# Optimization experiments

Hardware: AMD Instinct MI355X
Metric: run time of the kernel (lower is better)

The kernel has to match this reference:

```python
import jax, jax.numpy as jnp
import numpy as np

B, N, E, H = 4, 2048, 768, 8
D = E // H
SCALING = D ** (-0.5)


def setup_inputs() -> dict:
    key = jax.random.key(0)
    k0, k1, k2, k3, k4 = jax.random.split(key, 5)
    x = jax.random.normal(k0, (B, N, E), dtype=jnp.float32)
    Wqkv = jax.random.normal(k1, (E, 3 * E), dtype=jnp.float32) * 0.02
    bqkv = jax.random.normal(k2, (3 * E,), dtype=jnp.float32) * 0.02
    Wproj = jax.random.normal(k3, (E, E), dtype=jnp.float32) * 0.02
    bproj = jax.random.normal(k4, (E,), dtype=jnp.float32) * 0.02
    return {"x": x, "Wqkv": Wqkv, "bqkv": bqkv, "Wproj": Wproj, "bproj": bproj}


def reference(x, Wqkv, bqkv, Wproj, bproj):
    b, n, e = x.shape
    h, d = H, E // H
    # QKV projection: [b, n, 3e]
    qkv = x @ Wqkv + bqkv
    # rearrange 'b n (h d qkv) -> qkv b h n d': qkv is the INNERMOST axis
    qkv = qkv.reshape(b, n, h, d, 3)
    q = jnp.transpose(qkv[..., 0], (0, 2, 1, 3))  # [b, h, n, d]
    k = jnp.transpose(qkv[..., 1], (0, 2, 1, 3))
    v = jnp.transpose(qkv[..., 2], (0, 2, 1, 3))
    # unscaled attention scores, softmax, then post-softmax scaling (as in source)
    energy = jnp.einsum('bhqd,bhkd->bhqk', q, k)  # [b, h, n, n]
    att = jax.nn.softmax(energy, axis=-1) * SCALING
    out = jnp.einsum('bhqk,bhkd->bhqd', att, v)   # [b, h, n, d]
    out = jnp.transpose(out, (0, 2, 1, 3)).reshape(b, n, e)
    return out @ Wproj + bproj
```

## Files before the change

### kernel.cpp

```cpp
#include <hip/hip_runtime.h>
#include <cstdint>

#define BB 4
#define SEQ 2048
#define EMB 768
#define NH 8
#define HD 96
#define E3 2304
#define MTOK 8192
#define SCALING 0.10206207261596575f
#define LOG2E 1.44269504f

typedef unsigned short u16;
typedef unsigned int u32;
typedef __bf16 bf16x8 __attribute__((ext_vector_type(8)));
typedef float f32x4 __attribute__((ext_vector_type(4)));
typedef float f32x16 __attribute__((ext_vector_type(16)));

__device__ __forceinline__ u16 f2bf(float f) {
    union { float f; uint32_t u; } c; c.f = f;
    uint32_t u = c.u;
    return (u16)((u + 0x7FFFu + ((u >> 16) & 1u)) >> 16);
}
__device__ __forceinline__ u16 f2bf_fast(float f) {
    union { float f; uint32_t u; } c; c.f = f;
    return (u16)((c.u + 0x8000u) >> 16);
}
__device__ __forceinline__ uint32_t pk2(float a, float b) {
    return (uint32_t)f2bf(a) | ((uint32_t)f2bf(b) << 16);
}
__device__ __forceinline__ uint32_t pk2_fast(float a, float b) {
    return (uint32_t)f2bf_fast(a) | ((uint32_t)f2bf_fast(b) << 16);
}
__device__ __forceinline__ float fexp2(float x) {
    return __builtin_amdgcn_exp2f(x);
}
__device__ __forceinline__ void async16(const u16* g, u16* l) {
    __builtin_amdgcn_global_load_lds(
        (const __attribute__((address_space(1))) void*)g,
        (__attribute__((address_space(3))) void*)l, 16, 0, 0);
}


__global__ void cvt_x_kernel(const float* __restrict__ src, u16* __restrict__ dst, int n8) {
    int i = blockIdx.x * blockDim.x + threadIdx.x;
    if (i >= n8) return;
    const float4* s4 = (const float4*)src;
    float4 a = s4[2 * i];
    float4 c = s4[2 * i + 1];
    uint4 o;
    o.x = pk2(a.x, a.y); o.y = pk2(a.z, a.w);
    o.z = pk2(c.x, c.y); o.w = pk2(c.z, c.w);
    ((uint4*)dst)[i] = o;
}

__global__ __launch_bounds__(256) void transpose_w_kernel(const float* __restrict__ src,
                                                          u16* __restrict__ dst,
                                                          int ncols, int mode) {
    __shared__ float T[64][65];
    int j0 = blockIdx.x * 64, k0 = blockIdx.y * 64;
    int tid = threadIdx.x;
#pragma unroll
    for (int it = 0; it < 16; ++it) {
        int lin = it * 256 + tid;
        int rr2 = lin >> 6, jj = lin & 63;
        int j = j0 + jj;
        int c;
        if (mode == 0) c = j;
        else if (mode == 1) { int s = j / 768, rr = j % 768; c = (rr / 96) * 288 + (rr % 96) * 3 + s; }
        else { c = (j / 96) * 288 + (j % 96) * 3 + 2; }
        T[rr2][jj] = src[(k0 + rr2) * ncols + c];
    }
    __syncthreads();
#pragma unroll
    for (int it = 0; it < 16; ++it) {
        int lin = it * 256 + tid;
        int jr = lin >> 6, kc = lin & 63;
        dst[(size_t)(j0 + jr) * 768 + k0 + kc] = f2bf(T[kc][jr]);
    }
}


__device__ __forceinline__ void gemm_tiles(const u16* __restrict__ A,
                                           const u16* __restrict__ Bt,
                                           int m0, int n0, int tid,
                                           u16* As, u16* Bs, f32x4 acc[4][4]) {
    const int lane = tid & 63;
    const int w = tid >> 6;
    const int l15 = lane & 15;
    const int quad = lane >> 4;
    const int wr = (w >> 1) * 64;
    const int wc = (w & 1) * 64;
    const int swz = l15 & 7;
    for (int kb = 0; kb < 768; kb += 64) {
#pragma unroll
        for (int it = 0; it < 4; ++it) {
            int base = (w * 4 + it) * 64;
            int lin = base + lane;
            int row = lin >> 3, cl = lin & 7;
            int cg = cl ^ (row & 7);
            async16(&A[(size_t)(m0 + row) * 768 + kb + cg * 8], &As[base * 8]);
            async16(&Bt[(size_t)(n0 + row) * 768 + kb + cg * 8], &Bs[base * 8]);
        }
        __syncthreads();
#pragma unroll
        for (int ks = 0; ks < 2; ++ks) {
            bf16x8 af[4], bfg[4];
#pragma unroll
            for (int fi = 0; fi < 4; ++fi)
                af[fi] = *(const bf16x8*)&As[(wr + fi * 16 + l15) * 64 + (((ks * 4 + quad) ^ swz) * 8)];
#pragma unroll
            for (int fj = 0; fj < 4; ++fj)
                bfg[fj] = *(const bf16x8*)&Bs[(wc + fj * 16 + l15) * 64 + (((ks * 4 + quad) ^ swz) * 8)];
#pragma unroll
            for (int fi = 0; fi < 4; ++fi)
#pragma unroll
                for (int fj = 0; fj < 4; ++fj)
                    acc[fi][fj] = __builtin_amdgcn_mfma_f32_16x16x32_bf16(af[fi], bfg[fj], acc[fi][fj], 0, 0, 0);
        }
        __syncthreads();
    }
}

__global__ __launch_bounds__(256) void gemm_qk_kernel(const u16* __restrict__ A,
                                                      const u16* __restrict__ Bt,
                                                      const float* __restrict__ bqkv,
                                                      u16* __restrict__ qb,
                                                      u16* __restrict__ kg) {
    __shared__ __align__(16) u16 As[128 * 64];
    __shared__ __align__(16) u16 Bs[128 * 64];
    int tid = threadIdx.x;
    int n0 = blockIdx.x * 128, m0 = blockIdx.y * 128;
    f32x4 acc[4][4] = {};
    gemm_tiles(A, Bt, m0, n0, tid, As, Bs, acc);
    int lane = tid & 63, w = tid >> 6, l15 = lane & 15, quad = lane >> 4;
    int wr = (w >> 1) * 64, wc = (w & 1) * 64;
#pragma unroll
    for (int fj = 0; fj < 4; ++fj) {
        int j = n0 + wc + fj * 16 + l15;
        int s = j / 768, rr = j % 768;
        int hh = rr / 96, dd = rr % 96;
        float bv = bqkv[hh * 288 + dd * 3 + s];
#pragma unroll
        for (int fi = 0; fi < 4; ++fi) {
#pragma unroll
            for (int r = 0; r < 4; ++r) {
                int m = m0 + wr + fi * 16 + quad * 4 + r;
                int b = m >> 11, n = m & 2047;
                int bh = b * NH + hh;
                float v = acc[fi][fj][r] + bv;
                if (s == 0) {
                    qb[((size_t)bh * SEQ + n) * HD + dd] = f2bf(v * LOG2E);
                } else {
                    int cp = (dd >> 3) ^ (n & 7);
                    kg[((size_t)bh * SEQ + n) * 128 + cp * 8 + (dd & 7)] = f2bf(v);
                }
            }
        }
    }
}

__global__ __launch_bounds__(256) void gemm_v_kernel(const u16* __restrict__ A,
                                                     const u16* __restrict__ Bt,
                                                     const float* __restrict__ bqkv,
                                                     u16* __restrict__ vt) {
    __shared__ __align__(16) u16 As[128 * 64];
    __shared__ __align__(16) u16 Bs[128 * 64];
    int tid = threadIdx.x;
    int n0 = blockIdx.x * 128, m0 = blockIdx.y * 128;
    f32x4 acc[4][4] = {};
    gemm_tiles(A, Bt, m0, n0, tid, As, Bs, acc);
    int lane = tid & 63, w = tid >> 6, l15 = lane & 15, quad = lane >> 4;
    int wr = (w >> 1) * 64, wc = (w & 1) * 64;
    float bvs[4][4]; int hhs[4][4], dds[4][4];
#pragma unroll
    for (int fi = 0; fi < 4; ++fi)
#pragma unroll
        for (int r = 0; r < 4; ++r) {
            int m = m0 + wr + fi * 16 + quad * 4 + r;
            int hh = m / 96, dd = m % 96;
            hhs[fi][r] = hh; dds[fi][r] = dd;
            bvs[fi][r] = bqkv[hh * 288 + dd * 3 + 2];
        }
#pragma unroll
    for (int fj = 0; fj < 4; ++fj) {
        int n = n0 + wc + fj * 16 + l15;
        int b = n >> 11, nn = n & 2047;
#pragma unroll
        for (int fi = 0; fi < 4; ++fi) {
#pragma unroll
            for (int r = 0; r < 4; ++r) {
                int dd = dds[fi][r];
                int kk = (nn & ~63) | ((((nn >> 3) ^ dd) & 7) << 3) | (nn & 7);
                vt[((size_t)(b * NH + hhs[fi][r]) * HD + dd) * SEQ + kk] =
                    f2bf(acc[fi][fj][r] + bvs[fi][r]);
            }
        }
    }
}

__global__ __launch_bounds__(256) void gemm_proj_kernel(const u16* __restrict__ A,
                                                        const u16* __restrict__ Bt,
                                                        const float* __restrict__ bias,
                                                        float* __restrict__ out) {
    __shared__ __align__(16) u16 As[128 * 64];
    __shared__ __align__(16) u16 Bs[128 * 64];
    int tid = threadIdx.x;
    int n0 = blockIdx.x * 128, m0 = blockIdx.y * 128;
    f32x4 acc[4][4] = {};
    gemm_tiles(A, Bt, m0, n0, tid, As, Bs, acc);
    int lane = tid & 63, w = tid >> 6, l15 = lane & 15, quad = lane >> 4;
    int wr = (w >> 1) * 64, wc = (w & 1) * 64;
#pragma unroll
    for (int fj = 0; fj < 4; ++fj) {
        int j = n0 + wc + fj * 16 + l15;
        float bv = bias[j];
#pragma unroll
        for (int fi = 0; fi < 4; ++fi) {
#pragma unroll
            for (int r = 0; r < 4; ++r) {
                int m = m0 + wr + fi * 16 + quad * 4 + r;
                out[(size_t)m * 768 + j] = acc[fi][fj][r] + bv;
            }
        }
    }
}

__global__ __launch_bounds__(256) void attn_kernel(const u16* __restrict__ Q,
                                                   const u16* __restrict__ Kg,
                                                   const u16* __restrict__ Vt,
                                                   u16* __restrict__ AO) {
    __shared__ __align__(16) u16 Ks[2][64 * 128];
    __shared__ __align__(16) u16 Vs[2][96 * 64];
    int tid = threadIdx.x;
    int lane = tid & 63, w = tid >> 6;
    int l31 = lane & 31, hf = lane >> 5;
    int swz = l31 & 7;
    int qt = blockIdx.x, bh = blockIdx.y;
    int b = bh >> 3, head = bh & 7;
    const u16* qp = Q + (size_t)bh * SEQ * HD;
    const u16* kgp = Kg + (size_t)bh * SEQ * 128;
    const u16* vtp = Vt + (size_t)bh * HD * SEQ;
    int q0 = qt * 128 + w * 32;

    bf16x8 aq[6];
#pragma unroll
    for (int dc = 0; dc < 6; ++dc)
        aq[dc] = *(const bf16x8*)&qp[(size_t)(q0 + l31) * HD + dc * 16 + hf * 8];

    f32x16 Ot[3] = {};
    float lp = 0.f;

    auto stage = [&](int kt, int buf) {
        int k0 = kt * 64;
#pragma unroll
        for (int it = 0; it < 4; ++it) {
            int cw = w * 4 + it;
            async16(kgp + (size_t)(k0 + cw * 4 + (lane >> 4)) * 128 + (lane & 15) * 8,
                    &Ks[buf][cw * 512]);
        }
#pragma unroll
        for (int it = 0; it < 3; ++it) {
            int vw = w * 3 + it;
            async16(vtp + (size_t)(vw * 8 + (lane >> 3)) * SEQ + k0 + (lane & 7) * 8,
                    &Vs[buf][vw * 512]);
        }
    };

    stage(0, 0);
    __syncthreads();

    for (int kt = 0; kt < SEQ / 64; ++kt) {
        int cur = kt & 1;
        if (kt + 1 < SEQ / 64) stage(kt + 1, cur ^ 1);

        f32x16 Sv[2] = {};
#pragma unroll
        for (int tau = 0; tau < 2; ++tau) {
#pragma unroll
            for (int dc = 0; dc < 6; ++dc) {
                bf16x8 ka = *(const bf16x8*)&Ks[cur][(tau * 32 + l31) * 128 + (((2 * dc + hf) ^ swz) * 8)];
                Sv[tau] = __builtin_amdgcn_mfma_f32_32x32x16_bf16(ka, aq[dc], Sv[tau], 0, 0, 0);
            }
        }

        u32 pk[2][4][2];
#pragma unroll
        for (int tau = 0; tau < 2; ++tau)
#pragma unroll
            for (int g = 0; g < 4; ++g)
#pragma unroll
                for (int u = 0; u < 2; ++u) {
                    float p0 = fexp2(Sv[tau][g * 4 + 2 * u]);
                    float p1 = fexp2(Sv[tau][g * 4 + 2 * u + 1]);
                    lp += p0 + p1;
                    pk[tau][g][u] = pk2_fast(p0, p1);
                }
        u32 rv[2][2][2];
#pragma unroll
        for (int tau = 0; tau < 2; ++tau)
#pragma unroll
            for (int kc = 0; kc < 2; ++kc)
#pragma unroll
                for (int u = 0; u < 2; ++u) {
                    u32 send = hf ? pk[tau][2 * kc][u] : pk[tau][2 * kc + 1][u];
                    rv[tau][kc][u] = (u32)__shfl_xor((int)send, 32);
                }
#pragma unroll
        for (int tau = 0; tau < 2; ++tau) {
#pragma unroll
            for (int kc = 0; kc < 2; ++kc) {
                union { u32 u[4]; bf16x8 v; } pf;
                pf.u[0] = hf ? rv[tau][kc][0] : pk[tau][2 * kc][0];
                pf.u[1] = hf ? rv[tau][kc][1] : pk[tau][2 * kc][1];
                pf.u[2] = hf ? pk[tau][2 * kc + 1][0] : rv[tau][kc][0];
                pf.u[3] = hf ? pk[tau][2 * kc + 1][1] : rv[tau][kc][1];
#pragma unroll
                for (int t = 0; t < 3; ++t) {
                    bf16x8 va = *(const bf16x8*)&Vs[cur][(t * 32 + l31) * 64 + (((4 * tau + 2 * kc + hf) ^ swz) * 8)];
                    Ot[t] = __builtin_amdgcn_mfma_f32_32x32x16_bf16(va, pf.v, Ot[t], 0, 0, 0);
                }
            }
        }
        __syncthreads();
    }

    float l = lp + __shfl_xor(lp, 32);
    float sc = SCALING / l;
    int n = q0 + l31;
    size_t rowbase = ((size_t)b * SEQ + n) * EMB + head * HD;
#pragma unroll
    for (int t = 0; t < 3; ++t) {
#pragma unroll
        for (int g = 0; g < 4; ++g) {
            int d0 = t * 32 + 8 * g + 4 * hf;
            uint2 val;
            val.x = pk2(Ot[t][g * 4 + 0] * sc, Ot[t][g * 4 + 1] * sc);
            val.y = pk2(Ot[t][g * 4 + 2] * sc, Ot[t][g * 4 + 3] * sc);
            *(uint2*)&AO[rowbase + d0] = val;
        }
    }
}


extern "C" void kernel_launch(void* const* d_in, const int* in_sizes, int n_in,
                              void* d_out, int out_size, void* d_ws, size_t ws_size,
                              hipStream_t stream) {
    const float* x     = (const float*)d_in[0];
    const float* Wqkv  = (const float*)d_in[1];
    const float* bqkv  = (const float*)d_in[2];
    const float* Wproj = (const float*)d_in[3];
    const float* bproj = (const float*)d_in[4];
    float* out = (float*)d_out;

    char* p = (char*)d_ws;
    u16*   xb   = (u16*)p;  p += (size_t)MTOK * EMB * 2;
    u16*   wqkT = (u16*)p;  p += (size_t)1536 * EMB * 2;
    u16*   wvr  = (u16*)p;  p += (size_t)EMB * EMB * 2;
    u16*   wpt  = (u16*)p;  p += (size_t)EMB * EMB * 2;
    u16*   qb   = (u16*)p;  p += (size_t)MTOK * EMB * 2;
    u16*   kg   = (u16*)p;  p += (size_t)BB * NH * SEQ * 128 * 2;
    u16*   vt   = (u16*)p;  p += (size_t)MTOK * EMB * 2;
    u16*   ao   = (u16*)p;  p += (size_t)MTOK * EMB * 2;

    cvt_x_kernel<<<MTOK * EMB / 8 / 256, 256, 0, stream>>>(x, xb, MTOK * EMB / 8);
    transpose_w_kernel<<<dim3(1536 / 64, EMB / 64), 256, 0, stream>>>(Wqkv, wqkT, E3, 1);
    transpose_w_kernel<<<dim3(EMB / 64, EMB / 64), 256, 0, stream>>>(Wqkv, wvr, E3, 2);
    transpose_w_kernel<<<dim3(EMB / 64, EMB / 64), 256, 0, stream>>>(Wproj, wpt, EMB, 0);
    gemm_qk_kernel<<<dim3(1536 / 128, MTOK / 128), 256, 0, stream>>>(xb, wqkT, bqkv, qb, kg);
    gemm_v_kernel<<<dim3(MTOK / 128, EMB / 128), 256, 0, stream>>>(wvr, xb, bqkv, vt);
    attn_kernel<<<dim3(SEQ / 128, BB * NH), 256, 0, stream>>>(qb, kg, vt, ao);
    gemm_proj_kernel<<<dim3(EMB / 128, MTOK / 128), 256, 0, stream>>>(ao, wpt, bproj, out);
}
```

Before: 255.5 us.

## Split attention over key halves with combine pass, double query rows per warp

The attention kernel now handles 64 query rows per warp, so each K fragment load feeds two score MFMAs and each V load feeds two output MFMAs. The key range is split into two halves across blockIdx.z, giving a split-K flash layout whose bf16 partial outputs and row sums are merged and normalized by a new combine kernel. The V-projection and output-projection GEMMs move to 128x64 tiles to launch more blocks. The aim is higher LDS reuse and more parallelism in attention, at the cost of extra partial-output traffic, one more launch, and higher register pressure under launch_bounds(256,2).

```diff
diff --git a/kernel.cpp b/kernel.cpp
--- a/kernel.cpp
+++ b/kernel.cpp
@@ -8,6 +8,7 @@
 #define HD 96
 #define E3 2304
 #define MTOK 8192
+#define NROWS 65536
 #define SCALING 0.10206207261596575f
 #define LOG2E 1.44269504f
 
@@ -31,6 +32,9 @@
 }
 __device__ __forceinline__ uint32_t pk2_fast(float a, float b) {
     return (uint32_t)f2bf_fast(a) | ((uint32_t)f2bf_fast(b) << 16);
+}
+__device__ __forceinline__ float bf2f(u16 h) {
+    union { uint32_t u; float f; } c; c.u = ((uint32_t)h) << 16; return c.f;
 }
 __device__ __forceinline__ float fexp2(float x) {
     return __builtin_amdgcn_exp2f(x);
@@ -116,6 +120,54 @@
             for (int fi = 0; fi < 4; ++fi)
 #pragma unroll
                 for (int fj = 0; fj < 4; ++fj)
+                    acc[fi][fj] = __builtin_amdgcn_mfma_f32_16x16x32_bf16(af[fi], bfg[fj], acc[fi][fj], 0, 0, 0);
+        }
+        __syncthreads();
+    }
+}
+
+__device__ __forceinline__ void gemm_tiles64(const u16* __restrict__ A,
+                                             const u16* __restrict__ Bt,
+                                             int m0, int n0, int tid,
+                                             u16* As, u16* Bs, f32x4 acc[4][2]) {
+    const int lane = tid & 63;
+    const int w = tid >> 6;
+    const int l15 = lane & 15;
+    const int quad = lane >> 4;
+    const int wr = (w >> 1) * 64;
+    const int wc = (w & 1) * 32;
+    const int swz = l15 & 7;
+    for (int kb = 0; kb < 768; kb += 64) {
+#pragma unroll
+        for (int it = 0; it < 4; ++it) {
+            int base = (w * 4 + it) * 64;
+            int lin = base + lane;
+            int row = lin >> 3, cl = lin & 7;
+            int cg = cl ^ (row & 7);
+            async16(&A[(size_t)(m0 + row) * 768 + kb + cg * 8], &As[base * 8]);
+        }
+#pragma unroll
+        for (int it = 0; it < 2; ++it) {
+            int base = (w * 2 + it) * 64;
+            int lin = base + lane;
+            int row = lin >> 3, cl = lin & 7;
+            int cg = cl ^ (row & 7);
+            async16(&Bt[(size_t)(n0 + row) * 768 + kb + cg * 8], &Bs[base * 8]);
+        }
+        __syncthreads();
+#pragma unroll
+        for (int ks = 0; ks < 2; ++ks) {
+            bf16x8 af[4], bfg[2];
+#pragma unroll
+            for (int fi = 0; fi < 4; ++fi)
+                af[fi] = *(const bf16x8*)&As[(wr + fi * 16 + l15) * 64 + (((ks * 4 + quad) ^ swz) * 8)];
+#pragma unroll
+            for (int fj = 0; fj < 2; ++fj)
+                bfg[fj] = *(const bf16x8*)&Bs[(wc + fj * 16 + l15) * 64 + (((ks * 4 + quad) ^ swz) * 8)];
+#pragma unroll
+            for (int fi = 0; fi < 4; ++fi)
+#pragma unroll
+                for (int fj = 0; fj < 2; ++fj)
                     acc[fi][fj] = __builtin_amdgcn_mfma_f32_16x16x32_bf16(af[fi], bfg[fj], acc[fi][fj], 0, 0, 0);
         }
         __syncthreads();
@@ -165,13 +217,13 @@
                                                      const float* __restrict__ bqkv,
                                                      u16* __restrict__ vt) {
     __shared__ __align__(16) u16 As[128 * 64];
-    __shared__ __align__(16) u16 Bs[128 * 64];
+    __shared__ __align__(16) u16 Bs[64 * 64];
     int tid = threadIdx.x;
-    int n0 = blockIdx.x * 128, m0 = blockIdx.y * 128;
-    f32x4 acc[4][4] = {};
-    gemm_tiles(A, Bt, m0, n0, tid, As, Bs, acc);
+    int n0 = blockIdx.x * 64, m0 = blockIdx.y * 128;
+    f32x4 acc[4][2] = {};
+    gemm_tiles64(A, Bt, m0, n0, tid, As, Bs, acc);
     int lane = tid & 63, w = tid >> 6, l15 = lane & 15, quad = lane >> 4;
-    int wr = (w >> 1) * 64, wc = (w & 1) * 64;
+    int wr = (w >> 1) * 64, wc = (w & 1) * 32;
     float bvs[4][4]; int hhs[4][4], dds[4][4];
 #pragma unroll
     for (int fi = 0; fi < 4; ++fi)
@@ -183,7 +235,7 @@
             bvs[fi][r] = bqkv[hh * 288 + dd * 3 + 2];
         }
 #pragma unroll
-    for (int fj = 0; fj < 4; ++fj) {
+    for (int fj = 0; fj < 2; ++fj) {
         int n = n0 + wc + fj * 16 + l15;
         int b = n >> 11, nn = n & 2047;
 #pragma unroll
@@ -204,15 +256,15 @@
                                                         const float* __restrict__ bias,
                                                         float* __restrict__ out) {
     __shared__ __align__(16) u16 As[128 * 64];
-    __shared__ __align__(16) u16 Bs[128 * 64];
+    __shared__ __align__(16) u16 Bs[64 * 64];
     int tid = threadIdx.x;
-    int n0 = blockIdx.x * 128, m0 = blockIdx.y * 128;
-    f32x4 acc[4][4] = {};
-    gemm_tiles(A, Bt, m0, n0, tid, As, Bs, acc);
+    int n0 = blockIdx.x * 64, m0 = blockIdx.y * 128;
+    f32x4 acc[4][2] = {};
+    gemm_tiles64(A, Bt, m0, n0, tid, As, Bs, acc);
     int lane = tid & 63, w = tid >> 6, l15 = lane & 15, quad = lane >> 4;
-    int wr = (w >> 1) * 64, wc = (w & 1) * 64;
-#pragma unroll
-    for (int fj = 0; fj < 4; ++fj) {
+    int wr = (w >> 1) * 64, wc = (w & 1) * 32;
+#pragma unroll
+    for (int fj = 0; fj < 2; ++fj) {
         int j = n0 + wc + fj * 16 + l15;
         float bv = bias[j];
 #pragma unroll
@@ -226,33 +278,36 @@
     }
 }
 
-__global__ __launch_bounds__(256) void attn_kernel(const u16* __restrict__ Q,
-                                                   const u16* __restrict__ Kg,
-                                                   const u16* __restrict__ Vt,
-                                                   u16* __restrict__ AO) {
+__global__ __launch_bounds__(256, 2) void attn_kernel(const u16* __restrict__ Q,
+                                                      const u16* __restrict__ Kg,
+                                                      const u16* __restrict__ Vt,
+                                                      u16* __restrict__ part,
+                                                      float* __restrict__ lpart) {
     __shared__ __align__(16) u16 Ks[2][64 * 128];
     __shared__ __align__(16) u16 Vs[2][96 * 64];
     int tid = threadIdx.x;
     int lane = tid & 63, w = tid >> 6;
     int l31 = lane & 31, hf = lane >> 5;
     int swz = l31 & 7;
-    int qt = blockIdx.x, bh = blockIdx.y;
-    int b = bh >> 3, head = bh & 7;
+    int qt = blockIdx.x, bh = blockIdx.y, kh = blockIdx.z;
     const u16* qp = Q + (size_t)bh * SEQ * HD;
     const u16* kgp = Kg + (size_t)bh * SEQ * 128;
     const u16* vtp = Vt + (size_t)bh * HD * SEQ;
-    int q0 = qt * 128 + w * 32;
-
-    bf16x8 aq[6];
-#pragma unroll
-    for (int dc = 0; dc < 6; ++dc)
-        aq[dc] = *(const bf16x8*)&qp[(size_t)(q0 + l31) * HD + dc * 16 + hf * 8];
-
-    f32x16 Ot[3] = {};
-    float lp = 0.f;
+    int qbase = qt * 256 + w * 64;
+    int kbase = kh * 1024;
+
+    bf16x8 aq[2][6];
+#pragma unroll
+    for (int j = 0; j < 2; ++j)
+#pragma unroll
+        for (int dc = 0; dc < 6; ++dc)
+            aq[j][dc] = *(const bf16x8*)&qp[(size_t)(qbase + j * 32 + l31) * HD + dc * 16 + hf * 8];
+
+    f32x16 Ot[2][3] = {};
+    float lp[2] = {0.f, 0.f};
 
     auto stage = [&](int kt, int buf) {
-        int k0 = kt * 64;
+        int k0 = kbase + kt * 64;
 #pragma unroll
         for (int it = 0; it < 4; ++it) {
             int cw = w * 4 + it;
@@ -270,76 +325,108 @@
     stage(0, 0);
     __syncthreads();
 
-    for (int kt = 0; kt < SEQ / 64; ++kt) {
+    for (int kt = 0; kt < 16; ++kt) {
         int cur = kt & 1;
-        if (kt + 1 < SEQ / 64) stage(kt + 1, cur ^ 1);
-
-        f32x16 Sv[2] = {};
+        if (kt + 1 < 16) stage(kt + 1, cur ^ 1);
+
 #pragma unroll
         for (int tau = 0; tau < 2; ++tau) {
+            f32x16 Sv0 = {}, Sv1 = {};
 #pragma unroll
             for (int dc = 0; dc < 6; ++dc) {
                 bf16x8 ka = *(const bf16x8*)&Ks[cur][(tau * 32 + l31) * 128 + (((2 * dc + hf) ^ swz) * 8)];
-                Sv[tau] = __builtin_amdgcn_mfma_f32_32x32x16_bf16(ka, aq[dc], Sv[tau], 0, 0, 0);
-            }
-        }
-
-        u32 pk[2][4][2];
-#pragma unroll
-        for (int tau = 0; tau < 2; ++tau)
+                Sv0 = __builtin_amdgcn_mfma_f32_32x32x16_bf16(ka, aq[0][dc], Sv0, 0, 0, 0);
+                Sv1 = __builtin_amdgcn_mfma_f32_32x32x16_bf16(ka, aq[1][dc], Sv1, 0, 0, 0);
+            }
+            u32 pk[2][4][2];
 #pragma unroll
             for (int g = 0; g < 4; ++g)
 #pragma unroll
                 for (int u = 0; u < 2; ++u) {
-                    float p0 = fexp2(Sv[tau][g * 4 + 2 * u]);
-                    float p1 = fexp2(Sv[tau][g * 4 + 2 * u + 1]);
-                    lp += p0 + p1;
-                    pk[tau][g][u] = pk2_fast(p0, p1);
+                    float a0 = fexp2(Sv0[g * 4 + 2 * u]);
+                    float a1 = fexp2(Sv0[g * 4 + 2 * u + 1]);
+                    lp[0] += a0 + a1;
+                    pk[0][g][u] = pk2_fast(a0, a1);
+                    float b0 = fexp2(Sv1[g * 4 + 2 * u]);
+                    float b1 = fexp2(Sv1[g * 4 + 2 * u + 1]);
+                    lp[1] += b0 + b1;
+                    pk[1][g][u] = pk2_fast(b0, b1);
                 }
-        u32 rv[2][2][2];
-#pragma unroll
-        for (int tau = 0; tau < 2; ++tau)
-#pragma unroll
-            for (int kc = 0; kc < 2; ++kc)
-#pragma unroll
-                for (int u = 0; u < 2; ++u) {
-                    u32 send = hf ? pk[tau][2 * kc][u] : pk[tau][2 * kc + 1][u];
-                    rv[tau][kc][u] = (u32)__shfl_xor((int)send, 32);
-                }
-#pragma unroll
-        for (int tau = 0; tau < 2; ++tau) {
+            u32 rv[2][2][2];
+#pragma unroll
+            for (int j = 0; j < 2; ++j)
+#pragma unroll
+                for (int kc = 0; kc < 2; ++kc)
+#pragma unroll
+                    for (int u = 0; u < 2; ++u) {
+                        u32 send = hf ? pk[j][2 * kc][u] : pk[j][2 * kc + 1][u];
+                        rv[j][kc][u] = (u32)__shfl_xor((int)send, 32);
+                    }
 #pragma unroll
             for (int kc = 0; kc < 2; ++kc) {
-                union { u32 u[4]; bf16x8 v; } pf;
-                pf.u[0] = hf ? rv[tau][kc][0] : pk[tau][2 * kc][0];
-                pf.u[1] = hf ? rv[tau][kc][1] : pk[tau][2 * kc][1];
-                pf.u[2] = hf ? pk[tau][2 * kc + 1][0] : rv[tau][kc][0];
-                pf.u[3] = hf ? pk[tau][2 * kc + 1][1] : rv[tau][kc][1];
+                union { u32 u[4]; bf16x8 v; } pf0, pf1;
+                pf0.u[0] = hf ? rv[0][kc][0] : pk[0][2 * kc][0];
+                pf0.u[1] = hf ? rv[0][kc][1] : pk[0][2 * kc][1];
+                pf0.u[2] = hf ? pk[0][2 * kc + 1][0] : rv[0][kc][0];
+                pf0.u[3] = hf ? pk[0][2 * kc + 1][1] : rv[0][kc][1];
+                pf1.u[0] = hf ? rv[1][kc][0] : pk[1][2 * kc][0];
+                pf1.u[1] = hf ? rv[1][kc][1] : pk[1][2 * kc][1];
+                pf1.u[2] = hf ? pk[1][2 * kc + 1][0] : rv[1][kc][0];
+                pf1.u[3] = hf ? pk[1][2 * kc + 1][1] : rv[1][kc][1];
 #pragma unroll
                 for (int t = 0; t < 3; ++t) {
                     bf16x8 va = *(const bf16x8*)&Vs[cur][(t * 32 + l31) * 64 + (((4 * tau + 2 * kc + hf) ^ swz) * 8)];
-                    Ot[t] = __builtin_amdgcn_mfma_f32_32x32x16_bf16(va, pf.v, Ot[t], 0, 0, 0);
+                    Ot[0][t] = __builtin_amdgcn_mfma_f32_32x32x16_bf16(va, pf0.v, Ot[0][t], 0, 0, 0);
+                    Ot[1][t] = __builtin_amdgcn_mfma_f32_32x32x16_bf16(va, pf1.v, Ot[1][t], 0, 0, 0);
                 }
             }
         }
         __syncthreads();
     }
 
-    float l = lp + __shfl_xor(lp, 32);
+    size_t pb = (size_t)kh * NROWS + (size_t)bh * SEQ;
+#pragma unroll
+    for (int j = 0; j < 2; ++j) {
+        int q = qbase + j * 32 + l31;
+        float lr = lp[j] + __shfl_xor(lp[j], 32);
+        if (hf == 0) lpart[(size_t)kh * NROWS + (size_t)bh * SEQ + q] = lr;
+        size_t rowb = (pb + q) * HD;
+#pragma unroll
+        for (int t = 0; t < 3; ++t) {
+#pragma unroll
+            for (int g = 0; g < 4; ++g) {
+                int d0 = t * 32 + 8 * g + 4 * hf;
+                uint2 val;
+                val.x = pk2(Ot[j][t][g * 4 + 0], Ot[j][t][g * 4 + 1]);
+                val.y = pk2(Ot[j][t][g * 4 + 2], Ot[j][t][g * 4 + 3]);
+                *(uint2*)&part[rowb + d0] = val;
+            }
+        }
+    }
+}
+
+__global__ __launch_bounds__(256) void combine_kernel(const u16* __restrict__ part,
+                                                      const float* __restrict__ lpart,
+                                                      u16* __restrict__ ao) {
+    int idx = blockIdx.x * 256 + threadIdx.x;
+    int row = idx / 12, ch = idx % 12;
+    float l = lpart[row] + lpart[NROWS + row];
     float sc = SCALING / l;
-    int n = q0 + l31;
-    size_t rowbase = ((size_t)b * SEQ + n) * EMB + head * HD;
-#pragma unroll
-    for (int t = 0; t < 3; ++t) {
-#pragma unroll
-        for (int g = 0; g < 4; ++g) {
-            int d0 = t * 32 + 8 * g + 4 * hf;
-            uint2 val;
-            val.x = pk2(Ot[t][g * 4 + 0] * sc, Ot[t][g * 4 + 1] * sc);
-            val.y = pk2(Ot[t][g * 4 + 2] * sc, Ot[t][g * 4 + 3] * sc);
-            *(uint2*)&AO[rowbase + d0] = val;
-        }
-    }
+    const uint4 p0 = *(const uint4*)&part[(size_t)row * HD + ch * 8];
+    const uint4 p1 = *(const uint4*)&part[((size_t)NROWS + row) * HD + ch * 8];
+    const u16* a = (const u16*)&p0;
+    const u16* bq = (const u16*)&p1;
+    uint4 o;
+    u32* ou = (u32*)&o;
+#pragma unroll
+    for (int i = 0; i < 4; ++i) {
+        float e0 = (bf2f(a[2 * i]) + bf2f(bq[2 * i])) * sc;
+        float e1 = (bf2f(a[2 * i + 1]) + bf2f(bq[2 * i + 1])) * sc;
+        ou[i] = pk2(e0, e1);
+    }
+    int bh = row >> 11, n = row & 2047;
+    int b = bh >> 3, h = bh & 7;
+    *(uint4*)&ao[((size_t)(b * SEQ + n)) * EMB + h * HD + ch * 8] = o;
 }
 
 
@@ -354,21 +441,24 @@
     float* out = (float*)d_out;
 
     char* p = (char*)d_ws;
-    u16*   xb   = (u16*)p;  p += (size_t)MTOK * EMB * 2;
-    u16*   wqkT = (u16*)p;  p += (size_t)1536 * EMB * 2;
-    u16*   wvr  = (u16*)p;  p += (size_t)EMB * EMB * 2;
-    u16*   wpt  = (u16*)p;  p += (size_t)EMB * EMB * 2;
-    u16*   qb   = (u16*)p;  p += (size_t)MTOK * EMB * 2;
-    u16*   kg   = (u16*)p;  p += (size_t)BB * NH * SEQ * 128 * 2;
-    u16*   vt   = (u16*)p;  p += (size_t)MTOK * EMB * 2;
-    u16*   ao   = (u16*)p;  p += (size_t)MTOK * EMB * 2;
+    u16*   xb    = (u16*)p;  p += (size_t)MTOK * EMB * 2;
+    u16*   wqkT  = (u16*)p;  p += (size_t)1536 * EMB * 2;
+    u16*   wvr   = (u16*)p;  p += (size_t)EMB * EMB * 2;
+    u16*   wpt   = (u16*)p;  p += (size_t)EMB * EMB * 2;
+    u16*   qb    = (u16*)p;  p += (size_t)MTOK * EMB * 2;
+    u16*   kg    = (u16*)p;  p += (size_t)BB * NH * SEQ * 128 * 2;
+    u16*   vt    = (u16*)p;  p += (size_t)MTOK * EMB * 2;
+    u16*   ao    = (u16*)p;  p += (size_t)MTOK * EMB * 2;
+    u16*   partb = (u16*)p;  p += (size_t)2 * NROWS * HD * 2;
+    float* lpart = (float*)p; p += (size_t)2 * NROWS * 4;
 
     cvt_x_kernel<<<MTOK * EMB / 8 / 256, 256, 0, stream>>>(x, xb, MTOK * EMB / 8);
     transpose_w_kernel<<<dim3(1536 / 64, EMB / 64), 256, 0, stream>>>(Wqkv, wqkT, E3, 1);
     transpose_w_kernel<<<dim3(EMB / 64, EMB / 64), 256, 0, stream>>>(Wqkv, wvr, E3, 2);
     transpose_w_kernel<<<dim3(EMB / 64, EMB / 64), 256, 0, stream>>>(Wproj, wpt, EMB, 0);
     gemm_qk_kernel<<<dim3(1536 / 128, MTOK / 128), 256, 0, stream>>>(xb, wqkT, bqkv, qb, kg);
-    gemm_v_kernel<<<dim3(MTOK / 128, EMB / 128), 256, 0, stream>>>(wvr, xb, bqkv, vt);
-    attn_kernel<<<dim3(SEQ / 128, BB * NH), 256, 0, stream>>>(qb, kg, vt, ao);
-    gemm_proj_kernel<<<dim3(EMB / 128, MTOK / 128), 256, 0, stream>>>(ao, wpt, bproj, out);
-}
+    gemm_v_kernel<<<dim3(MTOK / 64, EMB / 128), 256, 0, stream>>>(wvr, xb, bqkv, vt);
+    attn_kernel<<<dim3(SEQ / 256, BB * NH, 2), 256, 0, stream>>>(qb, kg, vt, partb, lpart);
+    combine_kernel<<<NROWS * 12 / 256, 256, 0, stream>>>(partb, lpart, ao);
+    gemm_proj_kernel<<<dim3(EMB / 64, MTOK / 128), 256, 0, stream>>>(ao, wpt, bproj, out);
+}
```

After: 251.1 us. No clear change (-1.7%).
